# Kernel optimization log

Measured on AMD Instinct MI355X. Metric: run time of the kernel, lower is better.

The kernel has to match this reference:

```python
import jax, jax.numpy as jnp
import numpy as np

B, S, D = 2, 2048, 4096
H, KVH, HD = 32, 8, 128
WIN = 1024  # sliding window
THETA = 10000.0


def setup_inputs() -> dict:
    key = jax.random.key(0)
    ks = jax.random.split(key, 5)
    x = jax.random.normal(ks[0], (B, S, D), jnp.float32) * 0.02
    wq = jax.random.normal(ks[1], (H * HD, D), jnp.float32) * 0.02
    wk = jax.random.normal(ks[2], (KVH * HD, D), jnp.float32) * 0.02
    wv = jax.random.normal(ks[3], (KVH * HD, D), jnp.float32) * 0.02
    wo = jax.random.normal(ks[4], (D, H * HD), jnp.float32) * 0.02
    positions = jnp.arange(S, dtype=jnp.int32)
    inv_freq = 1.0 / (THETA ** (jnp.arange(0, HD, 2, dtype=jnp.float32) / HD))
    ang = positions.astype(jnp.float32)[:, None] * inv_freq[None, :]  # [S, HD/2]
    cos, sin = jnp.cos(ang), jnp.sin(ang)
    i = jnp.arange(S)[:, None]
    j = jnp.arange(S)[None, :]
    allowed = (j <= i) & (i - j < WIN)  # causal + sliding window
    mask = jnp.where(allowed, 0.0, -1e9).astype(jnp.float32)  # [S, S]
    return {"x": x, "wq": wq, "wk": wk, "wv": wv, "wo": wo,
            "cos": cos, "sin": sin, "mask": mask, "positions": positions}


def _apply_rope(t, cos, sin):
    # t: [B, S, nH, HD]; pairs are consecutive dims (torch view_as_complex layout)
    tr = t.reshape(t.shape[:-1] + (HD // 2, 2))
    t0, t1 = tr[..., 0], tr[..., 1]
    c = cos[None, :, None, :]
    s = sin[None, :, None, :]
    out = jnp.stack([t0 * c - t1 * s, t0 * s + t1 * c], axis=-1)
    return out.reshape(t.shape)


def reference(x, wq, wk, wv, wo, cos, sin, mask, positions):
    bsz, seqlen, _ = x.shape
    xq = (x @ wq.T).reshape(bsz, seqlen, H, HD)
    xk = (x @ wk.T).reshape(bsz, seqlen, KVH, HD)
    xv = (x @ wv.T).reshape(bsz, seqlen, KVH, HD)
    xq = _apply_rope(xq, cos, sin)
    xk = _apply_rope(xk, cos, sin)
    # GQA: repeat_kv head broadcast (prefill path: positions.size(0) > 1)
    rep = H // KVH
    key = jnp.repeat(xk, rep, axis=2)  # [B, S, H, HD]
    val = jnp.repeat(xv, rep, axis=2)
    q = xq.transpose(0, 2, 1, 3)  # [B, H, S, HD]
    k = key.transpose(0, 2, 1, 3)
    v = val.transpose(0, 2, 1, 3)
    scale = HD ** -0.5
    scores = jnp.einsum("bhqd,bhkd->bhqk", q, k) * scale
    scores = scores + mask[None, None, :, :]
    probs = jax.nn.softmax(scores.astype(jnp.float32), axis=-1).astype(q.dtype)
    out = jnp.einsum("bhqk,bhkd->bhqd", probs, v)
    out = out.transpose(0, 2, 1, 3).reshape(bsz, seqlen, H * HD)
    return out @ wo.T
```

## Files before the change

kernel.cpp:

```cpp
#include <hip/hip_runtime.h>
#include <hip/hip_bf16.h>

#define B_  2
#define S_  2048
#define D_  4096
#define H_  32
#define KVH_ 8
#define HD_ 128
#define WIN_ 1024

typedef __attribute__((ext_vector_type(8))) __bf16 bf16x8;
typedef __attribute__((ext_vector_type(4))) float f32x4;
using bf16 = __hip_bfloat16;

typedef const __attribute__((address_space(1))) void* gas_ptr;
typedef __attribute__((address_space(3))) void* las_ptr;

__device__ __forceinline__ void gload16(const void* g, void* l) {
    __builtin_amdgcn_global_load_lds((gas_ptr)g, (las_ptr)l, 16, 0, 0);
}

__device__ __forceinline__ bf16x8 load8(const bf16* p) {
    return *reinterpret_cast<const bf16x8*>(p);
}
__device__ __forceinline__ bf16x8 cvt8(const bf16* p) {
    return *reinterpret_cast<const bf16x8*>(p);
}
__device__ __forceinline__ bf16x8 cvt8(const float* p) {
    const float4* q = reinterpret_cast<const float4*>(p);
    float4 a = q[0], b = q[1];
    bf16x8 r;
    r[0] = (__bf16)a.x; r[1] = (__bf16)a.y; r[2] = (__bf16)a.z; r[3] = (__bf16)a.w;
    r[4] = (__bf16)b.x; r[5] = (__bf16)b.y; r[6] = (__bf16)b.z; r[7] = (__bf16)b.w;
    return r;
}
__device__ __forceinline__ void store1(float* p, float v) { *p = v; }
__device__ __forceinline__ void store1(bf16* p, float v) { *p = __float2bfloat16(v); }

#define GBAR()  __builtin_amdgcn_s_barrier()
#define SCB0()  __builtin_amdgcn_sched_barrier(0)
#define LGKM0() do { asm volatile("s_waitcnt lgkmcnt(0)" ::: "memory"); \
                     __builtin_amdgcn_sched_barrier(0); } while (0)
#define VMC(n)  do { asm volatile("s_waitcnt vmcnt(" #n ")" ::: "memory"); \
                     __builtin_amdgcn_sched_barrier(0); } while (0)

__global__ __launch_bounds__(256) void cast_kernel(const float* __restrict__ in,
                                                   bf16* __restrict__ out) {
    long i = ((long)blockIdx.x * 256 + threadIdx.x) * 8;
    const float4* p = reinterpret_cast<const float4*>(in + i);
    float4 a = p[0], b = p[1];
    bf16x8 r;
    r[0] = (__bf16)a.x; r[1] = (__bf16)a.y; r[2] = (__bf16)a.z; r[3] = (__bf16)a.w;
    r[4] = (__bf16)b.x; r[5] = (__bf16)b.y; r[6] = (__bf16)b.z; r[7] = (__bf16)b.w;
    *reinterpret_cast<bf16x8*>(out + i) = r;
}

template <typename TC>
__global__ __launch_bounds__(512, 2) void gemm_nt_256(
    const bf16* __restrict__ A, const bf16* __restrict__ Bm,
    TC* __restrict__ C, int M, int N, int K) {
    __shared__ __bf16 lds[2][2][256 * 64];

    const int tid  = threadIdx.x;
    const int wave = tid >> 6;
    const int lane = tid & 63;
    const int col  = lane & 15;
    const int quad = lane >> 4;
    const int c7   = col & 7;
    const int wmi  = wave >> 2;
    const int wni  = wave & 3;
    const long m0  = (long)blockIdx.y * 256;
    const long n0  = (long)blockIdx.x * 256;
    const int  nt  = K >> 6;

    f32x4 zero = {0.f, 0.f, 0.f, 0.f};
    f32x4 acc[8][4];
#pragma unroll
    for (int i = 0; i < 8; i++)
#pragma unroll
        for (int j = 0; j < 4; j++) acc[i][j] = zero;

    long gA[4], gB[4];
    int  lofs[4];
#pragma unroll
    for (int j = 0; j < 4; j++) {
        int r  = j * 64 + wave * 8 + (lane >> 3);
        int cg = (lane & 7) ^ (r & 7);
        gA[j]   = (m0 + r) * (long)K + cg * 8;
        gB[j]   = (n0 + r) * (long)K + cg * 8;
        lofs[j] = (j * 64 + wave * 8) * 128;
    }

#pragma unroll
    for (int j = 0; j < 4; j++) {
        gload16(A  + gA[j], (char*)lds[0][0] + lofs[j]);
        gload16(Bm + gB[j], (char*)lds[0][1] + lofs[j]);
    }
    if (nt > 1) {
#pragma unroll
        for (int j = 0; j < 4; j++)
            gload16(Bm + gB[j] + 64, (char*)lds[1][1] + lofs[j]);
        gload16(A + gA[0] + 64, (char*)lds[1][0] + lofs[0]);
        gload16(A + gA[2] + 64, (char*)lds[1][0] + lofs[2]);
        VMC(6);
    } else {
        VMC(0);
    }
    GBAR();

#define RDA_(dst, mf, ks) \
    dst = *reinterpret_cast<const bf16x8*>(Ab + (wmi * 128 + (mf) * 16 + col) * 128 \
                                              + ((((ks) << 2) + quad) ^ c7) * 16)
#define MFMA16(mb) \
    do { \
        _Pragma("unroll") \
        for (int ks = 0; ks < 2; ks++) { \
            _Pragma("unroll") \
            for (int nf = 0; nf < 4; nf++) { \
                acc[mb][nf]     = __builtin_amdgcn_mfma_f32_16x16x32_bf16( \
                    a[0][ks], bfr[nf][ks], acc[mb][nf], 0, 0, 0); \
                acc[mb + 1][nf] = __builtin_amdgcn_mfma_f32_16x16x32_bf16( \
                    a[1][ks], bfr[nf][ks], acc[mb + 1][nf], 0, 0, 0); \
            } \
        } \
    } while (0)

    for (int t = 0; t < nt; ++t) {
        const int cur = t & 1;
        const char* Ab = (const char*)lds[cur][0];
        const char* Bb = (const char*)lds[cur][1];
        char* An2 = (char*)lds[cur ^ 1][0];
        char* Ac2 = (char*)lds[cur][0];
        char* Bc2 = (char*)lds[cur][1];

        bf16x8 bfr[4][2];
#pragma unroll
        for (int nf = 0; nf < 4; nf++)
#pragma unroll
            for (int ks = 0; ks < 2; ks++)
                bfr[nf][ks] = *reinterpret_cast<const bf16x8*>(
                    Bb + (wni * 64 + nf * 16 + col) * 128 + (((ks << 2) + quad) ^ c7) * 16);
        bf16x8 a[2][2];
        RDA_(a[0][0], 0, 0); RDA_(a[0][1], 0, 1);
        RDA_(a[1][0], 1, 0); RDA_(a[1][1], 1, 1);
        if (t + 1 < nt) {
            long ko = (long)(t + 1) * 64;
            gload16(A + gA[1] + ko, An2 + lofs[1]);
            gload16(A + gA[3] + ko, An2 + lofs[3]);
        }
        GBAR();
        LGKM0();
        __builtin_amdgcn_s_setprio(1);
        MFMA16(0);
        __builtin_amdgcn_s_setprio(0);
        GBAR();

        RDA_(a[0][0], 2, 0); RDA_(a[0][1], 2, 1);
        RDA_(a[1][0], 3, 0); RDA_(a[1][1], 3, 1);
        if (t + 2 < nt) {
            long ko = (long)(t + 2) * 64;
#pragma unroll
            for (int j = 0; j < 4; j++)
                gload16(Bm + gB[j] + ko, Bc2 + lofs[j]);
        }
        GBAR();
        LGKM0();
        __builtin_amdgcn_s_setprio(1);
        MFMA16(2);
        __builtin_amdgcn_s_setprio(0);
        GBAR();

        RDA_(a[0][0], 4, 0); RDA_(a[0][1], 4, 1);
        RDA_(a[1][0], 5, 0); RDA_(a[1][1], 5, 1);
        if (t + 2 < nt) {
            long ko = (long)(t + 2) * 64;
            gload16(A + gA[0] + ko, Ac2 + lofs[0]);
            gload16(A + gA[2] + ko, Ac2 + lofs[2]);
        }
        GBAR();
        LGKM0();
        __builtin_amdgcn_s_setprio(1);
        MFMA16(4);
        __builtin_amdgcn_s_setprio(0);
        GBAR();

        RDA_(a[0][0], 6, 0); RDA_(a[0][1], 6, 1);
        RDA_(a[1][0], 7, 0); RDA_(a[1][1], 7, 1);
        LGKM0();
        __builtin_amdgcn_s_setprio(1);
        MFMA16(6);
        __builtin_amdgcn_s_setprio(0);
        if (t + 2 < nt) { VMC(6); } else { VMC(0); }
        GBAR();
    }

#pragma unroll
    for (int mf = 0; mf < 8; mf++) {
#pragma unroll
        for (int nf = 0; nf < 4; nf++) {
            long row = m0 + wmi * 128 + mf * 16 + quad * 4;
            long cc  = n0 + wni * 64 + nf * 16 + col;
#pragma unroll
            for (int r = 0; r < 4; r++)
                store1(&C[(row + r) * (long)N + cc], acc[mf][nf][r]);
        }
    }
}

template <typename TC>
__global__ __launch_bounds__(256) void gemm_nt_fast(
    const bf16* __restrict__ A, const bf16* __restrict__ Bm,
    TC* __restrict__ C, int M, int N, int K) {
    __shared__ __bf16 As[128 * 64];
    __shared__ __bf16 Bs[128 * 64];

    const int tid  = threadIdx.x;
    const int wave = tid >> 6;
    const int lane = tid & 63;
    const int col  = lane & 15;
    const int quad = lane >> 4;
    const int c7   = col & 7;
    const int wm   = (wave >> 1) * 64;
    const int wn   = (wave & 1) * 64;
    const long m0  = (long)blockIdx.y * 128;
    const long n0  = (long)blockIdx.x * 128;

    f32x4 zero = {0.f, 0.f, 0.f, 0.f};
    f32x4 acc[4][4];
#pragma unroll
    for (int i = 0; i < 4; i++)
#pragma unroll
        for (int j = 0; j < 4; j++) acc[i][j] = zero;

    long goffA[4], goffB[4];
    int  loff[4];
#pragma unroll
    for (int i = 0; i < 4; i++) {
        int r  = (wave * 4 + i) * 8 + (lane >> 3);
        int cg = (lane & 7) ^ (r & 7);
        goffA[i] = (m0 + r) * (long)K + cg * 8;
        goffB[i] = (n0 + r) * (long)K + cg * 8;
        loff[i]  = (wave * 4 + i) * 1024;
    }

    for (int kt = 0; kt < K; kt += 64) {
#pragma unroll
        for (int i = 0; i < 4; i++) {
            gload16(A + goffA[i] + kt, (char*)As + loff[i]);
            gload16(Bm + goffB[i] + kt, (char*)Bs + loff[i]);
        }
        __syncthreads();

        bf16x8 af[2][4], bfv[2][4];
#pragma unroll
        for (int ks = 0; ks < 2; ks++) {
#pragma unroll
            for (int mt = 0; mt < 4; mt++) {
                int row = wm + mt * 16 + col;
                af[ks][mt] = *reinterpret_cast<const bf16x8*>(
                    (const char*)As + row * 128 + (((ks << 2) + quad) ^ c7) * 16);
            }
#pragma unroll
            for (int nt = 0; nt < 4; nt++) {
                int row = wn + nt * 16 + col;
                bfv[ks][nt] = *reinterpret_cast<const bf16x8*>(
                    (const char*)Bs + row * 128 + (((ks << 2) + quad) ^ c7) * 16);
            }
        }
#pragma unroll
        for (int ks = 0; ks < 2; ks++)
#pragma unroll
            for (int mt = 0; mt < 4; mt++)
#pragma unroll
                for (int nt = 0; nt < 4; nt++)
                    acc[mt][nt] = __builtin_amdgcn_mfma_f32_16x16x32_bf16(
                        af[ks][mt], bfv[ks][nt], acc[mt][nt], 0, 0, 0);
        __syncthreads();
    }

#pragma unroll
    for (int mt = 0; mt < 4; mt++) {
#pragma unroll
        for (int nt = 0; nt < 4; nt++) {
            long row = m0 + wm + mt * 16 + quad * 4;
            long cc  = n0 + wn + nt * 16 + col;
#pragma unroll
            for (int r = 0; r < 4; r++)
                store1(&C[(row + r) * (long)N + cc], acc[mt][nt][r]);
        }
    }
}

template <typename TA, typename TB, typename TC>
__global__ __launch_bounds__(256) void gemm_nt(
    const TA* __restrict__ A, const TB* __restrict__ Bm,
    TC* __restrict__ C, int M, int N, int K) {
    __shared__ __bf16 As[128 * 40];
    __shared__ __bf16 Bs[128 * 40];

    const int tid  = threadIdx.x;
    const int wave = tid >> 6;
    const int lane = tid & 63;
    const int col  = lane & 15;
    const int quad = lane >> 4;
    const int wm   = (wave >> 1) * 64;
    const int wn   = (wave & 1) * 64;
    const long m0  = (long)blockIdx.y * 128;
    const long n0  = (long)blockIdx.x * 128;

    f32x4 zero = {0.f, 0.f, 0.f, 0.f};
    f32x4 acc[4][4];
#pragma unroll
    for (int i = 0; i < 4; i++)
#pragma unroll
        for (int j = 0; j < 4; j++) acc[i][j] = zero;

    const int srow = tid >> 2;
    const int sch  = (tid & 3) * 8;

    for (int kt = 0; kt < K; kt += 32) {
        bf16x8 av0 = cvt8(A + (m0 + srow)      * (long)K + kt + sch);
        bf16x8 av1 = cvt8(A + (m0 + srow + 64) * (long)K + kt + sch);
        bf16x8 bv0 = cvt8(Bm + (n0 + srow)      * (long)K + kt + sch);
        bf16x8 bv1 = cvt8(Bm + (n0 + srow + 64) * (long)K + kt + sch);
        *reinterpret_cast<bf16x8*>(&As[srow * 40 + sch])        = av0;
        *reinterpret_cast<bf16x8*>(&As[(srow + 64) * 40 + sch]) = av1;
        *reinterpret_cast<bf16x8*>(&Bs[srow * 40 + sch])        = bv0;
        *reinterpret_cast<bf16x8*>(&Bs[(srow + 64) * 40 + sch]) = bv1;
        __syncthreads();

        bf16x8 af[4], bfv[4];
#pragma unroll
        for (int mt = 0; mt < 4; mt++)
            af[mt] = *reinterpret_cast<const bf16x8*>(&As[(wm + mt * 16 + col) * 40 + quad * 8]);
#pragma unroll
        for (int nt = 0; nt < 4; nt++)
            bfv[nt] = *reinterpret_cast<const bf16x8*>(&Bs[(wn + nt * 16 + col) * 40 + quad * 8]);
#pragma unroll
        for (int mt = 0; mt < 4; mt++)
#pragma unroll
            for (int nt = 0; nt < 4; nt++)
                acc[mt][nt] = __builtin_amdgcn_mfma_f32_16x16x32_bf16(
                    af[mt], bfv[nt], acc[mt][nt], 0, 0, 0);
        __syncthreads();
    }

#pragma unroll
    for (int mt = 0; mt < 4; mt++) {
#pragma unroll
        for (int nt = 0; nt < 4; nt++) {
            long row = m0 + wm + mt * 16 + quad * 4;
            long cc  = n0 + wn + nt * 16 + col;
#pragma unroll
            for (int r = 0; r < 4; r++)
                store1(&C[(row + r) * (long)N + cc], acc[mt][nt][r]);
        }
    }
}

__global__ void rope_kernel(bf16* __restrict__ t, const float* __restrict__ cosb,
                            const float* __restrict__ sinb, int nh, int total) {
    int idx = blockIdx.x * blockDim.x + threadIdx.x;
    if (idx >= total) return;
    int pair = idx & 63;
    int rest = idx >> 6;
    int hh   = rest % nh;
    int tok  = rest / nh;
    int s    = tok & (S_ - 1);
    long base = (long)tok * (nh * HD_) + hh * HD_ + pair * 2;
    float c  = cosb[s * 64 + pair];
    float sn = sinb[s * 64 + pair];
    float t0 = __bfloat162float(t[base]);
    float t1 = __bfloat162float(t[base + 1]);
    t[base]     = __float2bfloat16(t0 * c - t1 * sn);
    t[base + 1] = __float2bfloat16(t0 * sn + t1 * c);
}

__global__ __launch_bounds__(256) void transpose_v(const bf16* __restrict__ v,
                                                   bf16* __restrict__ vt) {
    __shared__ __bf16 tile[64][72];
    const int s0 = blockIdx.x * 64;
    const int d0 = blockIdx.y * 64;
    const int b  = blockIdx.z;
    const int tid = threadIdx.x;
    const int tr  = tid >> 3;
    const int c8  = (tid & 7) * 8;
#pragma unroll
    for (int p = 0; p < 2; p++) {
        int srow = tr + p * 32;
        bf16x8 val = load8(v + ((long)(b * S_ + s0 + srow)) * 1024 + d0 + c8);
        *reinterpret_cast<bf16x8*>(&tile[srow][c8]) = val;
    }
    __syncthreads();
#pragma unroll
    for (int p = 0; p < 2; p++) {
        int dd = tr + p * 32;
        bf16x8 ov;
#pragma unroll
        for (int j = 0; j < 8; j++) ov[j] = tile[c8 + j][dd];
        *reinterpret_cast<bf16x8*>(vt + ((long)(b * 1024 + d0 + dd)) * S_ + s0 + c8) = ov;
    }
}

__global__ __launch_bounds__(256) void attn_kernel(
    const bf16* __restrict__ q, const bf16* __restrict__ k,
    const bf16* __restrict__ vt, bf16* __restrict__ o) {
    const int qb  = blockIdx.x;
    const int h   = blockIdx.y;
    const int b   = blockIdx.z;
    const int tid = threadIdx.x;
    const int wave = tid >> 6;
    const int lane = tid & 63;
    const int col  = lane & 15;
    const int quad = lane >> 4;
    const int kvh  = h >> 2;
    const int i0   = qb * 64;
    const float scale = 0.08838834764831845f;

    __shared__ __bf16 Ks[2][64 * 128];
    __shared__ __bf16 Vs[2][128 * 64];
    __shared__ __bf16 Pl[4][16 * 72];

    bf16x8 qa[4];
    const bf16* qptr = q + ((long)(b * S_ + i0 + wave * 16 + col)) * (H_ * HD_)
                         + h * HD_ + quad * 8;
#pragma unroll
    for (int ks = 0; ks < 4; ks++) qa[ks] = load8(qptr + ks * 32);

    long gK[4], gV[4];
    int  lK[4], lV[4];
#pragma unroll
    for (int i = 0; i < 4; i++) {
        int rK  = (wave * 4 + i) * 4 + (lane >> 4);
        int cgK = (lane & 15) ^ (rK & 15);
        gK[i] = ((long)(b * S_) + rK) * (KVH_ * HD_) + kvh * HD_ + cgK * 8;
        lK[i] = (wave * 4 + i) * 1024;
        int rV  = (wave * 4 + i) * 8 + (lane >> 3);
        int cgV = (lane & 7) ^ (rV & 7);
        gV[i] = ((long)(b * 1024) + kvh * HD_ + rV) * (long)S_ + cgV * 8;
        lV[i] = (wave * 4 + i) * 1024;
    }

    f32x4 zero = {0.f, 0.f, 0.f, 0.f};
    f32x4 oacc[8];
#pragma unroll
    for (int i = 0; i < 8; i++) oacc[i] = zero;
    float lsum[4] = {0.f, 0.f, 0.f, 0.f};

    const int kb0 = (qb >= 16) ? (qb - 16) : 0;

    VMC(0);

#pragma unroll
    for (int i = 0; i < 4; i++) {
        gload16(k + gK[i] + (long)kb0 * 64 * (KVH_ * HD_), (char*)Ks[0] + lK[i]);
        gload16(vt + gV[i] + kb0 * 64, (char*)Vs[0] + lV[i]);
    }

    for (int kb = kb0; kb <= qb; kb++) {
        const int cur = (kb - kb0) & 1;
        if (kb < qb) {
#pragma unroll
            for (int i = 0; i < 4; i++) {
                gload16(k + gK[i] + (long)(kb + 1) * 64 * (KVH_ * HD_),
                        (char*)Ks[cur ^ 1] + lK[i]);
                gload16(vt + gV[i] + (kb + 1) * 64, (char*)Vs[cur ^ 1] + lV[i]);
            }
            VMC(8);
        } else {
            VMC(0);
        }
        GBAR();
        SCB0();

        f32x4 sfr[4];
        __builtin_amdgcn_s_setprio(1);
#pragma unroll
        for (int nt = 0; nt < 4; nt++) {
            f32x4 s = zero;
            int row = nt * 16 + col;
#pragma unroll
            for (int ks = 0; ks < 4; ks++) {
                bf16x8 bfv = *reinterpret_cast<const bf16x8*>(
                    (const char*)Ks[cur] + row * 256 + (((ks << 2) + quad) ^ col) * 16);
                s = __builtin_amdgcn_mfma_f32_16x16x32_bf16(qa[ks], bfv, s, 0, 0, 0);
            }
            sfr[nt] = s;
        }
        __builtin_amdgcn_s_setprio(0);
#pragma unroll
        for (int nt = 0; nt < 4; nt++) {
            int j = kb * 64 + nt * 16 + col;
#pragma unroll
            for (int r = 0; r < 4; r++) {
                int i = i0 + wave * 16 + quad * 4 + r;
                float p = 0.f;
                if (j <= i && (i - j) < WIN_) p = __expf(sfr[nt][r] * scale);
                lsum[r] += p;
                Pl[wave][(quad * 4 + r) * 72 + nt * 16 + col] = __float2bfloat16(p);
            }
        }
        __builtin_amdgcn_s_setprio(1);
#pragma unroll
        for (int ks2 = 0; ks2 < 2; ks2++) {
            bf16x8 pa = *reinterpret_cast<const bf16x8*>(
                &Pl[wave][col * 72 + ks2 * 32 + quad * 8]);
#pragma unroll
            for (int nt2 = 0; nt2 < 8; nt2++) {
                int d = nt2 * 16 + col;
                bf16x8 vb = *reinterpret_cast<const bf16x8*>(
                    (const char*)Vs[cur] + d * 128 + ((((ks2 << 2) + quad)) ^ (col & 7)) * 16);
                oacc[nt2] = __builtin_amdgcn_mfma_f32_16x16x32_bf16(
                    pa, vb, oacc[nt2], 0, 0, 0);
            }
        }
        __builtin_amdgcn_s_setprio(0);
        GBAR();
        SCB0();
    }

#pragma unroll
    for (int m = 1; m < 16; m <<= 1) {
#pragma unroll
        for (int r = 0; r < 4; r++) lsum[r] += __shfl_xor(lsum[r], m, 64);
    }

    bf16* op = o + ((long)(b * S_ + i0 + wave * 16 + quad * 4)) * (H_ * HD_) + h * HD_;
#pragma unroll
    for (int nt2 = 0; nt2 < 8; nt2++) {
#pragma unroll
        for (int r = 0; r < 4; r++)
            op[(long)r * (H_ * HD_) + nt2 * 16 + col] =
                __float2bfloat16(oacc[nt2][r] / lsum[r]);
    }
}

extern "C" void kernel_launch(void* const* d_in, const int* in_sizes, int n_in,
                              void* d_out, int out_size, void* d_ws, size_t ws_size,
                              hipStream_t stream) {
    const float* x    = (const float*)d_in[0];
    const float* wq   = (const float*)d_in[1];
    const float* wk   = (const float*)d_in[2];
    const float* wv   = (const float*)d_in[3];
    const float* wo   = (const float*)d_in[4];
    const float* cosb = (const float*)d_in[5];
    const float* sinb = (const float*)d_in[6];
    float* out = (float*)d_out;

    const size_t T   = (size_t)B_ * S_;
    const size_t SZ_D  = T * (H_ * HD_);
    const size_t SZ_KV = T * (KVH_ * HD_);

    dim3 blk(256);
    const size_t need_fast = (SZ_D * 3 + SZ_KV * 3 + SZ_D) * 2;

    if (ws_size >= need_fast) {
        bf16* xb    = (bf16*)d_ws;
        bf16* wbuf  = xb    + SZ_D;
        bf16* q_ws  = wbuf  + SZ_D;
        bf16* k_ws  = q_ws  + SZ_D;
        bf16* v_ws  = k_ws  + SZ_KV;
        bf16* vt_ws = v_ws  + SZ_KV;
        bf16* ao_ws = vt_ws + SZ_KV;

        cast_kernel<<<SZ_D / 2048, blk, 0, stream>>>(x, xb);
        cast_kernel<<<SZ_D / 2048, blk, 0, stream>>>(wq, wbuf);
        gemm_nt_256<bf16><<<dim3(16, 16), dim3(512), 0, stream>>>(xb, wbuf, q_ws, 4096, 4096, 4096);
        cast_kernel<<<SZ_KV / 2048, blk, 0, stream>>>(wk, wbuf);
        gemm_nt_fast<bf16><<<dim3(8, 32), blk, 0, stream>>>(xb, wbuf, k_ws, 4096, 1024, 4096);
        cast_kernel<<<SZ_KV / 2048, blk, 0, stream>>>(wv, wbuf);
        gemm_nt_fast<bf16><<<dim3(8, 32), blk, 0, stream>>>(xb, wbuf, v_ws, 4096, 1024, 4096);

        rope_kernel<<<(B_ * S_ * H_ * 64 + 255) / 256, blk, 0, stream>>>(
            q_ws, cosb, sinb, H_, B_ * S_ * H_ * 64);
        rope_kernel<<<(B_ * S_ * KVH_ * 64 + 255) / 256, blk, 0, stream>>>(
            k_ws, cosb, sinb, KVH_, B_ * S_ * KVH_ * 64);
        transpose_v<<<dim3(32, 16, 2), blk, 0, stream>>>(v_ws, vt_ws);

        attn_kernel<<<dim3(32, 32, 2), blk, 0, stream>>>(q_ws, k_ws, vt_ws, ao_ws);

        cast_kernel<<<SZ_D / 2048, blk, 0, stream>>>(wo, wbuf);
        gemm_nt_256<float><<<dim3(16, 16), dim3(512), 0, stream>>>(ao_ws, wbuf, out, 4096, 4096, 4096);
    } else {
        bf16* q_ws  = (bf16*)d_ws;
        bf16* k_ws  = q_ws  + SZ_D;
        bf16* v_ws  = k_ws  + SZ_KV;
        bf16* vt_ws = v_ws  + SZ_KV;
        bf16* ao_ws = vt_ws + SZ_KV;

        gemm_nt<float, float, bf16><<<dim3(32, 32), blk, 0, stream>>>(x, wq, q_ws, 4096, 4096, 4096);
        gemm_nt<float, float, bf16><<<dim3(8, 32),  blk, 0, stream>>>(x, wk, k_ws, 4096, 1024, 4096);
        gemm_nt<float, float, bf16><<<dim3(8, 32),  blk, 0, stream>>>(x, wv, v_ws, 4096, 1024, 4096);

        rope_kernel<<<(B_ * S_ * H_ * 64 + 255) / 256, blk, 0, stream>>>(
            q_ws, cosb, sinb, H_, B_ * S_ * H_ * 64);
        rope_kernel<<<(B_ * S_ * KVH_ * 64 + 255) / 256, blk, 0, stream>>>(
            k_ws, cosb, sinb, KVH_, B_ * S_ * KVH_ * 64);
        transpose_v<<<dim3(32, 16, 2), blk, 0, stream>>>(v_ws, vt_ws);

        attn_kernel<<<dim3(32, 32, 2), blk, 0, stream>>>(q_ws, k_ws, vt_ws, ao_ws);

        gemm_nt<bf16, float, float><<<dim3(32, 32), blk, 0, stream>>>(ao_ws, wo, out, 4096, 4096, 4096);
    }
}
```

Measured before the change: 794.3 us.

## Stage K/V tiles through registers into single LDS buffer instead of double-buffered direct loads

Replaces the double-buffered global_load_lds prefetch of K and V tiles with a register-staged prefetch. Each iteration writes the previously loaded registers into a single LDS buffer, then issues global loads for the next tile into registers, which overlap with the MFMA work. This halves the K/V shared memory footprint, which may raise occupancy. The cost is extra VGPRs, explicit LDS stores, and an additional barrier per iteration.

After: 788.0 us. No clear change (-0.8%).

```diff
diff --git a/kernel.cpp b/kernel.cpp
--- a/kernel.cpp
+++ b/kernel.cpp
@@ -417,8 +417,8 @@
     const int i0   = qb * 64;
     const float scale = 0.08838834764831845f;
 
-    __shared__ __bf16 Ks[2][64 * 128];
-    __shared__ __bf16 Vs[2][128 * 64];
+    __shared__ __bf16 Ks[64 * 128];
+    __shared__ __bf16 Vs[128 * 64];
     __shared__ __bf16 Pl[4][16 * 72];
 
     bf16x8 qa[4];
@@ -449,29 +449,34 @@
 
     const int kb0 = (qb >= 16) ? (qb - 16) : 0;
 
-    VMC(0);
-
+    bf16x8 kreg[4], vreg[4];
 #pragma unroll
     for (int i = 0; i < 4; i++) {
-        gload16(k + gK[i] + (long)kb0 * 64 * (KVH_ * HD_), (char*)Ks[0] + lK[i]);
-        gload16(vt + gV[i] + kb0 * 64, (char*)Vs[0] + lV[i]);
+        kreg[i] = *reinterpret_cast<const bf16x8*>(k + gK[i] + (long)kb0 * 64 * (KVH_ * HD_));
+        vreg[i] = *reinterpret_cast<const bf16x8*>(vt + gV[i] + kb0 * 64);
     }
 
     for (int kb = kb0; kb <= qb; kb++) {
-        const int cur = (kb - kb0) & 1;
+        GBAR();
+        SCB0();
+#pragma unroll
+        for (int i = 0; i < 4; i++) {
+            *reinterpret_cast<bf16x8*>((char*)Ks + lK[i] + lane * 16) = kreg[i];
+            *reinterpret_cast<bf16x8*>((char*)Vs + lV[i] + lane * 16) = vreg[i];
+        }
+        LGKM0();
+        GBAR();
+        SCB0();
         if (kb < qb) {
 #pragma unroll
             for (int i = 0; i < 4; i++) {
-                gload16(k + gK[i] + (long)(kb + 1) * 64 * (KVH_ * HD_),
-                        (char*)Ks[cur ^ 1] + lK[i]);
-                gload16(vt + gV[i] + (kb + 1) * 64, (char*)Vs[cur ^ 1] + lV[i]);
+                kreg[i] = *reinterpret_cast<const bf16x8*>(
+                    k + gK[i] + (long)(kb + 1) * 64 * (KVH_ * HD_));
+                vreg[i] = *reinterpret_cast<const bf16x8*>(
+                    vt + gV[i] + (kb + 1) * 64);
             }
-            VMC(8);
-        } else {
-            VMC(0);
-        }
-        GBAR();
-        SCB0();
+            SCB0();
+        }
 
         f32x4 sfr[4];
         __builtin_amdgcn_s_setprio(1);
@@ -482,7 +487,7 @@
 #pragma unroll
             for (int ks = 0; ks < 4; ks++) {
                 bf16x8 bfv = *reinterpret_cast<const bf16x8*>(
-                    (const char*)Ks[cur] + row * 256 + (((ks << 2) + quad) ^ col) * 16);
+                    (const char*)Ks + row * 256 + (((ks << 2) + quad) ^ col) * 16);
                 s = __builtin_amdgcn_mfma_f32_16x16x32_bf16(qa[ks], bfv, s, 0, 0, 0);
             }
             sfr[nt] = s;
@@ -509,14 +514,12 @@
             for (int nt2 = 0; nt2 < 8; nt2++) {
                 int d = nt2 * 16 + col;
                 bf16x8 vb = *reinterpret_cast<const bf16x8*>(
-                    (const char*)Vs[cur] + d * 128 + ((((ks2 << 2) + quad)) ^ (col & 7)) * 16);
+                    (const char*)Vs + d * 128 + ((((ks2 << 2) + quad)) ^ (col & 7)) * 16);
                 oacc[nt2] = __builtin_amdgcn_mfma_f32_16x16x32_bf16(
                     pa, vb, oacc[nt2], 0, 0, 0);
             }
         }
         __builtin_amdgcn_s_setprio(0);
-        GBAR();
-        SCB0();
     }
 
 #pragma unroll
```
